# Optimization experiments

Hardware: AMD Instinct MI355X
Metric: run time of the kernel (lower is better)

The kernel has to match this reference:

```python
import jax, jax.numpy as jnp
import numpy as np

C = 1024          # analysis_channels
K = 2             # encoder kernel_size
DILATIONS = (1, 2, 4, 8, 16, 32, 64, 1)
N_EVENTS = 16
N_FREQS = 16
NEG_SLOPE = 0.2   # leaky_relu slope
B, T = 64, 128    # batch, spectrogram frames (n_samples=2**15, hop 256)
WINIT = 0.05      # exp.init_weights uniform(-0.05, 0.05)
POS_CH = 2 * N_FREQS + 1  # 33


def setup_inputs() -> dict:
    key = jax.random.key(0)
    ks = jax.random.split(key, 8)
    u = lambda k, shape: jax.random.uniform(k, shape, jnp.float32, -WINIT, WINIT)
    return {
        'x': jax.random.normal(ks[0], (B, C, T), jnp.float32),  # pre-computed spectrogram path
        'w_spec': u(ks[1], (C, C)), 'b_spec': jnp.zeros((C,), jnp.float32),
        'w_pos': u(ks[2], (C, POS_CH)), 'b_pos': jnp.zeros((C,), jnp.float32),
        'enc_w': u(ks[3], (len(DILATIONS), C, C, K)), 'enc_b': jnp.zeros((len(DILATIONS), C), jnp.float32),
        'w_vec': u(ks[4], (C, C)), 'b_vec': jnp.zeros((C,), jnp.float32),
        'w_sw': u(ks[5], (1, C)), 'b_sw': jnp.zeros((1,), jnp.float32),
        'w_par': u(ks[6], (57, C)), 'b_par': jnp.zeros((57,), jnp.float32),
    }


def _pos_encoded(batch, time):
    # [ramp, sin(2^i * ramp), cos(2^i * ramp) for i in range(16)] -> 33 channels
    pos = jnp.linspace(-1.0, 1.0, time)[:, None]
    feats = [pos]
    for i in range(N_FREQS):
        feats.append(jnp.sin((2.0 ** i) * pos))
        feats.append(jnp.cos((2.0 ** i) * pos))
    p = jnp.concatenate(feats, axis=-1).T  # [33, T]
    return jnp.broadcast_to(p[None], (batch, POS_CH, time))


def _forward(x, w_spec, b_spec, w_pos, b_pos, enc_w, enc_b,
             w_vec, b_vec, w_sw, b_sw, w_par, b_par):
    batch, _, time = x.shape
    pos = _pos_encoded(batch, time)
    pos = jnp.einsum('oc,bct->bot', w_pos, pos) + b_pos[None, :, None]
    h = jnp.einsum('oc,bct->bot', w_spec, x) + b_spec[None, :, None] + pos

    # AntiCausalStack: residual dilated blocks, right (anti-causal) padding, summed skip outputs
    acc = jnp.zeros_like(h)
    for i, d in enumerate(DILATIONS):
        skip = h
        hp = jnp.pad(h, ((0, 0), (0, 0), (0, d * (K - 1))))  # pad end -> anti-causal
        conv = jax.lax.conv_general_dilated(
            hp, enc_w[i], (1,), [(0, 0)], rhs_dilation=(d,),
            dimension_numbers=('NCH', 'OIH', 'NCH')) + enc_b[i][None, :, None]
        conv = jnp.where(conv >= 0, conv, NEG_SLOPE * conv)  # leaky_relu
        h = conv + skip
        # do_norm=True: unit-norm over channel dim per time step
        h = h / (jnp.linalg.norm(h, axis=1, keepdims=True) + 1e-8)
        acc = acc + h
    encoded = acc

    vecs = jnp.einsum('oc,bct->bot', w_vec, encoded) + b_vec[None, :, None]    # [B,C,T]
    switch = jnp.einsum('oc,bct->bot', w_sw, encoded) + b_sw[None, :, None]    # [B,1,T]
    attn = jnp.abs(switch)[:, 0, :]                                             # [B,T]

    # sparsify + sparsify_vectors: top-k event scores, gather vectors, scale by score
    values, indices = jax.lax.top_k(attn, N_EVENTS)                             # [B,16]
    gathered = jnp.take_along_axis(vecs, indices[:, None, :], axis=2)           # [B,C,16]
    events = gathered.transpose(0, 2, 1) * values[:, :, None]                   # [B,16,C]

    return jnp.einsum('bnc,pc->bnp', events, w_par) + b_par[None, None, :]      # [B,16,57]


def reference(x, w_spec, b_spec, w_pos, b_pos, enc_w, enc_b,
              w_vec, b_vec, w_sw, b_sw, w_par, b_par):
    return _forward(x, w_spec, b_spec, w_pos, b_pos, enc_w, enc_b,
                    w_vec, b_vec, w_sw, b_sw, w_par, b_par)
```

## Files before the change

kernel.cpp:

```cpp
#include <hip/hip_runtime.h>
#include <math.h>

#define kB 64
#define kC 1024
#define kT 128
#define kLayers 8
#define kPos 33
#define kEv 16
#define kPar 57

#define BM 128
#define kOB (kC / BM)
#define BK 16
#define NTHR 256

#define SLAB ((size_t)kB * kC * kT)

typedef __attribute__((ext_vector_type(8))) short short8v;
typedef __attribute__((ext_vector_type(4))) float float4v;
typedef __attribute__((ext_vector_type(4))) unsigned short ushort4v;

__device__ __forceinline__ unsigned short bf_hi(float f) {
    unsigned int x = __float_as_uint(f);
    unsigned int r = x + 0x7fffu + ((x >> 16) & 1u);
    return (unsigned short)(r >> 16);
}
__device__ __forceinline__ float bf_f(unsigned short u) {
    return __uint_as_float(((unsigned int)u) << 16);
}

__global__ void pos_kernel(const float* __restrict__ w_pos,
                           const float* __restrict__ b_pos,
                           float* __restrict__ posproj) {
    int o = blockIdx.x;
    int t = threadIdx.x;
    float ramp = -1.0f + 2.0f * (float)t / (float)(kT - 1);
    const float* wr = w_pos + (size_t)o * kPos;
    float s = b_pos[o] + wr[0] * ramp;
    float p2 = 1.0f;
#pragma unroll
    for (int i = 0; i < 16; ++i) {
        float sv, cv;
        sincosf(p2 * ramp, &sv, &cv);
        s += wr[1 + 2 * i] * sv + wr[2 + 2 * i] * cv;
        p2 *= 2.0f;
    }
    posproj[(size_t)o * kT + t] = s;
}

__global__ void mt_kernel(const float* __restrict__ w_par,
                          const float* __restrict__ w_vec,
                          const float* __restrict__ b_vec,
                          float* __restrict__ Mt,
                          float* __restrict__ pbias) {
    if (blockIdx.x == kPar) {
        int p = threadIdx.x;
        if (p < kPar) {
            float s = 0.f;
            for (int c = 0; c < kC; ++c) s += w_par[(size_t)p * kC + c] * b_vec[c];
            pbias[p] = s;
        }
        return;
    }
    int p = blockIdx.x;
    int k = threadIdx.x * 4;
    float mx = 0.f, my = 0.f, mz = 0.f, mw = 0.f;
    for (int o = 0; o < kC; ++o) {
        float wp = w_par[(size_t)p * kC + o];
        float4 wv = *(const float4*)(w_vec + (size_t)o * kC + k);
        mx += wp * wv.x; my += wp * wv.y; mz += wp * wv.z; mw += wp * wv.w;
    }
    Mt[(size_t)(k + 0) * kPar + p] = mx;
    Mt[(size_t)(k + 1) * kPar + p] = my;
    Mt[(size_t)(k + 2) * kPar + p] = mz;
    Mt[(size_t)(k + 3) * kPar + p] = mw;
}

__global__ __launch_bounds__(NTHR) void spec_gemm(
    const float* __restrict__ x, const float* __restrict__ w_spec,
    const float* __restrict__ b_spec, const float* __restrict__ posproj,
    float* __restrict__ h) {
    __shared__ float As[BK][BM];
    __shared__ float Bs[BK][kT];
    const int obase = blockIdx.x * BM;
    const int b = blockIdx.y;
    const int tid = threadIdx.x;
    const int tx4 = (tid & 15) * 4;
    const int ty4 = (tid >> 4) * 4;
    const float* xb = x + (size_t)b * kC * kT;
    float acc[8][8] = {};

    for (int kc = 0; kc < kC; kc += BK) {
        __syncthreads();
        {
            int oo = tid >> 1;
            int ccb = (tid & 1) * 8;
            const float* wrow = w_spec + (size_t)(obase + oo) * kC + kc + ccb;
            float4 v0 = *(const float4*)(wrow);
            float4 v1 = *(const float4*)(wrow + 4);
            As[ccb + 0][oo] = v0.x; As[ccb + 1][oo] = v0.y;
            As[ccb + 2][oo] = v0.z; As[ccb + 3][oo] = v0.w;
            As[ccb + 4][oo] = v1.x; As[ccb + 5][oo] = v1.y;
            As[ccb + 6][oo] = v1.z; As[ccb + 7][oo] = v1.w;
        }
#pragma unroll
        for (int pass = 0; pass < 2; ++pass) {
            int row = (tid >> 5) + pass * 8;
            int col = (tid & 31) * 4;
            *(float4*)&Bs[row][col] = *(const float4*)(xb + (size_t)(kc + row) * kT + col);
        }
        __syncthreads();
#pragma unroll
        for (int kk = 0; kk < BK; ++kk) {
            float a[8], bb[8];
            *(float4*)&a[0] = *(float4*)&As[kk][ty4];
            *(float4*)&a[4] = *(float4*)&As[kk][64 + ty4];
            *(float4*)&bb[0] = *(float4*)&Bs[kk][tx4];
            *(float4*)&bb[4] = *(float4*)&Bs[kk][64 + tx4];
#pragma unroll
            for (int m = 0; m < 8; ++m)
#pragma unroll
                for (int n = 0; n < 8; ++n) acc[m][n] += a[m] * bb[n];
        }
    }
#pragma unroll
    for (int m = 0; m < 8; ++m) {
        int o = obase + (m < 4 ? ty4 + m : 64 + ty4 + m - 4);
        float bias = b_spec[o];
        const float* pp = posproj + (size_t)o * kT;
        float* hrow = h + ((size_t)b * kC + o) * kT;
#pragma unroll
        for (int half = 0; half < 2; ++half) {
            int t0 = half * 64 + tx4;
            float4 pv = *(const float4*)(pp + t0);
            float4 r;
            r.x = acc[m][half * 4 + 0] + bias + pv.x;
            r.y = acc[m][half * 4 + 1] + bias + pv.y;
            r.z = acc[m][half * 4 + 2] + bias + pv.z;
            r.w = acc[m][half * 4 + 3] + bias + pv.w;
            *(float4*)(hrow + t0) = r;
        }
    }
}

__global__ void wconv_kernel(const float* __restrict__ src,
                             unsigned short* __restrict__ wpl) {
    int o = blockIdx.x;
    int tid = threadIdx.x;
    const float* r = src + (size_t)o * (2 * kC) + tid * 8;
    float4 v0 = *(const float4*)r;
    float4 v1 = *(const float4*)(r + 4);
    float t0v[4] = {v0.x, v0.z, v1.x, v1.z};
    float t1v[4] = {v0.y, v0.w, v1.y, v1.w};
    int c0 = tid * 4;
    ushort4v h0, l0, h1, l1;
#pragma unroll
    for (int j = 0; j < 4; ++j) {
        unsigned short h = bf_hi(t0v[j]); h0[j] = h; l0[j] = bf_hi(t0v[j] - bf_f(h));
        unsigned short g = bf_hi(t1v[j]); h1[j] = g; l1[j] = bf_hi(t1v[j] - bf_f(g));
    }
    size_t base = (size_t)o * kC + c0;
    const size_t P = (size_t)kC * kC;
    *(ushort4v*)&wpl[base] = h0;
    *(ushort4v*)&wpl[base + P] = h1;
    *(ushort4v*)&wpl[base + 2 * P] = l0;
    *(ushort4v*)&wpl[base + 3 * P] = l1;
}

template <int DIL>
__global__ __launch_bounds__(NTHR, 2) void conv_mfma(
    const unsigned short* __restrict__ tpl,
    const unsigned short* __restrict__ wpl,
    const float* __restrict__ bconv,
    float* __restrict__ hpre,
    float* __restrict__ ssp) {
    __shared__ short Asl[2 * 128 * 64];
    __shared__ short Bsl[192 * 64];
    __shared__ float red[1024];
    const int tid = threadIdx.x;
    const int obase = blockIdx.x * BM;
    const int b = blockIdx.y;
    const int lane = tid & 63;
    const int w = tid >> 6;
    const int r16 = lane & 15;
    const int kq = lane >> 4;
    const int mrow = (w & 1) * 64;
    const int ncol = (w >> 1) * 64;
    const size_t PW = (size_t)kC * kC;

    float4v acc[4][4];
#pragma unroll
    for (int m = 0; m < 4; ++m)
#pragma unroll
        for (int n = 0; n < 4; ++n) {
            float4v z = {0.f, 0.f, 0.f, 0.f};
            acc[m][n] = z;
        }

    {
        short8v z = {0, 0, 0, 0, 0, 0, 0, 0};
#pragma unroll
        for (int r = 0; r < 2; ++r) {
            int cw = r * 256 + tid;
            int t = 128 + (cw >> 3);
            int g = cw & 7;
            *(short8v*)&Bsl[t * 64 + ((g ^ (t & 7)) << 3)] = z;
        }
    }

    for (int kc = 0; kc < kC; kc += 32) {
        __syncthreads();
#pragma unroll
        for (int r = 0; r < 8; ++r) {
            int cw = r * 256 + tid;
            int g = cw & 7;
            int o = (cw >> 3) & 127;
            int tap = cw >> 10;
            size_t src = ((size_t)((g & 1) * 2 + tap) * kC + (obase + o)) * kC + kc + ((g >> 1) << 3);
            short8v v = *(const short8v*)&wpl[src];
            *(short8v*)&Asl[tap * 8192 + o * 64 + ((g ^ (o & 7)) << 3)] = v;
        }
#pragma unroll
        for (int r = 0; r < 4; ++r) {
            int cw = r * 256 + tid;
            int g = cw & 7;
            int t = cw >> 3;
            size_t src = (size_t)(g & 1) * SLAB + ((size_t)b * kT + t) * kC + kc + ((g >> 1) << 3);
            short8v v = *(const short8v*)&tpl[src];
            *(short8v*)&Bsl[t * 64 + ((g ^ (t & 7)) << 3)] = v;
        }
        __syncthreads();
#pragma unroll
        for (int tap = 0; tap < 2; ++tap) {
            short8v ah[4], al[4], bh[4], bl[4];
#pragma unroll
            for (int m = 0; m < 4; ++m) {
                int ol = mrow + m * 16 + r16;
                const short* rowp = &Asl[tap * 8192 + ol * 64];
                ah[m] = *(const short8v*)&rowp[(((kq << 1)) ^ (ol & 7)) << 3];
                al[m] = *(const short8v*)&rowp[(((kq << 1) | 1) ^ (ol & 7)) << 3];
            }
#pragma unroll
            for (int n = 0; n < 4; ++n) {
                int tr = ncol + n * 16 + r16 + tap * DIL;
                const short* rowp = &Bsl[tr * 64];
                bh[n] = *(const short8v*)&rowp[(((kq << 1)) ^ (tr & 7)) << 3];
                bl[n] = *(const short8v*)&rowp[(((kq << 1) | 1) ^ (tr & 7)) << 3];
            }
#pragma unroll
            for (int m = 0; m < 4; ++m)
#pragma unroll
                for (int n = 0; n < 4; ++n) {
                    acc[m][n] = __builtin_amdgcn_mfma_f32_16x16x32_bf16(ah[m], bh[n], acc[m][n], 0, 0, 0);
                    acc[m][n] = __builtin_amdgcn_mfma_f32_16x16x32_bf16(ah[m], bl[n], acc[m][n], 0, 0, 0);
                    acc[m][n] = __builtin_amdgcn_mfma_f32_16x16x32_bf16(al[m], bh[n], acc[m][n], 0, 0, 0);
                }
        }
    }

    const unsigned short* thi = tpl;
    const unsigned short* tlo = tpl + SLAB;
    float sn[4] = {0.f, 0.f, 0.f, 0.f};
#pragma unroll
    for (int m = 0; m < 4; ++m) {
        int ob4 = obase + mrow + m * 16 + kq * 4;
        float4v bias = *(const float4v*)&bconv[ob4];
#pragma unroll
        for (int n = 0; n < 4; ++n) {
            int t = ncol + n * 16 + r16;
            size_t sidx = ((size_t)b * kT + t) * kC + ob4;
            ushort4v sh = *(const ushort4v*)&thi[sidx];
            ushort4v sl = *(const ushort4v*)&tlo[sidx];
#pragma unroll
            for (int j = 0; j < 4; ++j) {
                float v = acc[m][n][j] + bias[j];
                v = v >= 0.f ? v : 0.2f * v;
                float hp = v + bf_f(sh[j]) + bf_f(sl[j]);
                hpre[((size_t)b * kC + ob4 + j) * kT + t] = hp;
                sn[n] += hp * hp;
            }
        }
    }
#pragma unroll
    for (int n = 0; n < 4; ++n)
        red[w * 256 + kq * 64 + n * 16 + r16] = sn[n];
    __syncthreads();
    if (tid < kT) {
        int t = tid;
        int base = (t < 64) ? 0 : 2;
        int tl = t & 63;
        float s = 0.f;
#pragma unroll
        for (int ww = 0; ww < 2; ++ww)
#pragma unroll
            for (int q = 0; q < 4; ++q)
                s += red[(base + ww) * 256 + q * 64 + tl];
        ssp[((size_t)blockIdx.x * kB + b) * kT + t] = s;
    }
}

__global__ void normfac(const float* __restrict__ ssp, float* __restrict__ rn) {
    int b = blockIdx.x;
    int t = threadIdx.x;
    float s = 0.f;
#pragma unroll
    for (int j = 0; j < kOB; ++j) s += ssp[((size_t)j * kB + b) * kT + t];
    rn[b * kT + t] = 1.0f / (sqrtf(s) + 1e-8f);
}

template <int MODE>
__global__ void trans_kernel(const float* __restrict__ hsrc,
                             const float* __restrict__ rn,
                             float* __restrict__ acc,
                             unsigned short* __restrict__ tpl,
                             int first) {
    __shared__ float tile[64][68];
    int b = blockIdx.x;
    int c0 = blockIdx.y * 64;
    int t0 = blockIdx.z * 64;
    int tid = threadIdx.x;
#pragma unroll
    for (int r = 0; r < 4; ++r) {
        int row = r * 16 + (tid >> 4);
        int col = (tid & 15) * 4;
        size_t idx = ((size_t)b * kC + c0 + row) * kT + t0 + col;
        float4 v = *(const float4*)&hsrc[idx];
        if constexpr (MODE) {
            float4 rv = *(const float4*)&rn[b * kT + t0 + col];
            v.x *= rv.x; v.y *= rv.y; v.z *= rv.z; v.w *= rv.w;
            if (first) {
                *(float4*)&acc[idx] = v;
            } else {
                float4 a = *(const float4*)&acc[idx];
                a.x += v.x; a.y += v.y; a.z += v.z; a.w += v.w;
                *(float4*)&acc[idx] = a;
            }
        }
        *(float4*)&tile[row][col] = v;
    }
    __syncthreads();
    unsigned short* thi = tpl;
    unsigned short* tlo = tpl + SLAB;
#pragma unroll
    for (int r = 0; r < 2; ++r) {
        int trow = r * 32 + (tid >> 3);
        int cc = (tid & 7) * 8;
        short8v hp, lp;
#pragma unroll
        for (int j = 0; j < 8; ++j) {
            float f = tile[cc + j][trow];
            unsigned short h = bf_hi(f);
            hp[j] = (short)h;
            lp[j] = (short)bf_hi(f - bf_f(h));
        }
        size_t dst = ((size_t)b * kT + t0 + trow) * kC + c0 + cc;
        *(short8v*)&thi[dst] = hp;
        *(short8v*)&tlo[dst] = lp;
    }
}

__global__ void switch_partial(const float* __restrict__ acc,
                               const float* __restrict__ w_sw,
                               float* __restrict__ swp) {
    int b = blockIdx.x;
    int cblk = blockIdx.y;
    int t = threadIdx.x & 127;
    int half = threadIdx.x >> 7;
    int cbase = cblk * 128 + half * 64;
    const float* arow = acc + ((size_t)b * kC + cbase) * kT + t;
    float p = 0.f;
    for (int j = 0; j < 64; ++j) p += w_sw[cbase + j] * arow[(size_t)j * kT];
    __shared__ float red2[2][128];
    red2[half][t] = p;
    __syncthreads();
    if (half == 0)
        swp[((size_t)cblk * kB + b) * kT + t] = red2[0][t] + red2[1][t];
}

__global__ void topk_kernel(const float* __restrict__ swp,
                            const float* __restrict__ b_sw,
                            float* __restrict__ vals, int* __restrict__ idxs) {
    int b = blockIdx.x;
    int t = threadIdx.x;
    __shared__ float cur[128];
    __shared__ float rv[128];
    __shared__ int ri[128];
    {
        float s = b_sw[0];
#pragma unroll
        for (int j = 0; j < kC / 128; ++j)
            s += swp[((size_t)j * kB + b) * kT + t];
        cur[t] = fabsf(s);
    }
    __syncthreads();
    for (int r = 0; r < kEv; ++r) {
        rv[t] = cur[t];
        ri[t] = t;
        __syncthreads();
        for (int s = 64; s >= 1; s >>= 1) {
            if (t < s) {
                float v2 = rv[t + s];
                int i2 = ri[t + s];
                if (v2 > rv[t] || (v2 == rv[t] && i2 < ri[t])) { rv[t] = v2; ri[t] = i2; }
            }
            __syncthreads();
        }
        if (t == 0) {
            vals[b * kEv + r] = rv[0];
            idxs[b * kEv + r] = ri[0];
            cur[ri[0]] = -1.0f;
        }
        __syncthreads();
    }
}

__global__ void final_kernel(const float* __restrict__ acc,
                             const float* __restrict__ Mt,
                             const float* __restrict__ pbias,
                             const float* __restrict__ b_par,
                             const float* __restrict__ vals,
                             const int* __restrict__ idxs,
                             float* __restrict__ out) {
    int bn = blockIdx.x;
    int b = bn >> 4;
    int tid = threadIdx.x;
    __shared__ float gs[kC];
    __shared__ float redf[4][64];
    int idx = idxs[bn];
    float val = vals[bn];
#pragma unroll
    for (int j = 0; j < 4; ++j) {
        int k = tid * 4 + j;
        gs[k] = acc[((size_t)b * kC + k) * kT + idx];
    }
    __syncthreads();
    int kg = tid >> 6;
    int pp = tid & 63;
    float partial = 0.f;
    if (pp < kPar) {
        for (int j = 0; j < 256; ++j) {
            int k = kg * 256 + j;
            partial += Mt[(size_t)k * kPar + pp] * gs[k];
        }
    }
    redf[kg][pp] = partial;
    __syncthreads();
    if (kg == 0 && pp < kPar) {
        float s = redf[0][pp] + redf[1][pp] + redf[2][pp] + redf[3][pp];
        out[(size_t)bn * kPar + pp] = val * (s + pbias[pp]) + b_par[pp];
    }
}

extern "C" void kernel_launch(void* const* d_in, const int* in_sizes, int n_in,
                              void* d_out, int out_size, void* d_ws, size_t ws_size,
                              hipStream_t stream) {
    (void)in_sizes; (void)n_in; (void)out_size; (void)ws_size;
    const float* x      = (const float*)d_in[0];
    const float* w_spec = (const float*)d_in[1];
    const float* b_spec = (const float*)d_in[2];
    const float* w_pos  = (const float*)d_in[3];
    const float* b_pos  = (const float*)d_in[4];
    const float* enc_w  = (const float*)d_in[5];
    const float* enc_b  = (const float*)d_in[6];
    const float* w_vec  = (const float*)d_in[7];
    const float* b_vec  = (const float*)d_in[8];
    const float* w_sw   = (const float*)d_in[9];
    const float* b_sw   = (const float*)d_in[10];
    const float* w_par  = (const float*)d_in[11];
    const float* b_par  = (const float*)d_in[12];
    float* out = (float*)d_out;

    float* hpre = (float*)d_ws;
    float* acc  = hpre + SLAB;
    unsigned short* tpl = (unsigned short*)(acc + SLAB);
    unsigned short* wpl = tpl + 2 * SLAB;
    float* posproj = (float*)(wpl + (size_t)4 * kC * kC);
    float* ssp   = posproj + (size_t)kC * kT;
    float* rnorm = ssp + (size_t)kOB * kB * kT;
    float* swp   = rnorm + (size_t)kB * kT;
    float* vals  = swp + (size_t)kOB * kB * kT;
    int*   idxs  = (int*)(vals + kB * kEv);
    float* Mt    = (float*)(idxs + kB * kEv);
    float* pbias = Mt + (size_t)kC * kPar;

    pos_kernel<<<kC, kT, 0, stream>>>(w_pos, b_pos, posproj);
    mt_kernel<<<kPar + 1, 256, 0, stream>>>(w_par, w_vec, b_vec, Mt, pbias);
    spec_gemm<<<dim3(kC / BM, kB), NTHR, 0, stream>>>(x, w_spec, b_spec, posproj, hpre);
    trans_kernel<0><<<dim3(kB, kC / 64, kT / 64), NTHR, 0, stream>>>(
        hpre, rnorm, acc, tpl, 0);

    const int dils[kLayers] = {1, 2, 4, 8, 16, 32, 64, 1};
    for (int i = 0; i < kLayers; ++i) {
        const float* wi = enc_w + (size_t)i * kC * kC * 2;
        const float* bi = enc_b + (size_t)i * kC;
        wconv_kernel<<<kC, NTHR, 0, stream>>>(wi, wpl);
        dim3 grid(kC / BM, kB);
        switch (dils[i]) {
            case 1:  conv_mfma<1><<<grid, NTHR, 0, stream>>>(tpl, wpl, bi, hpre, ssp); break;
            case 2:  conv_mfma<2><<<grid, NTHR, 0, stream>>>(tpl, wpl, bi, hpre, ssp); break;
            case 4:  conv_mfma<4><<<grid, NTHR, 0, stream>>>(tpl, wpl, bi, hpre, ssp); break;
            case 8:  conv_mfma<8><<<grid, NTHR, 0, stream>>>(tpl, wpl, bi, hpre, ssp); break;
            case 16: conv_mfma<16><<<grid, NTHR, 0, stream>>>(tpl, wpl, bi, hpre, ssp); break;
            case 32: conv_mfma<32><<<grid, NTHR, 0, stream>>>(tpl, wpl, bi, hpre, ssp); break;
            case 64: conv_mfma<64><<<grid, NTHR, 0, stream>>>(tpl, wpl, bi, hpre, ssp); break;
        }
        normfac<<<kB, kT, 0, stream>>>(ssp, rnorm);
        trans_kernel<1><<<dim3(kB, kC / 64, kT / 64), NTHR, 0, stream>>>(
            hpre, rnorm, acc, tpl, i == 0 ? 1 : 0);
    }

    switch_partial<<<dim3(kB, kC / 128), 256, 0, stream>>>(acc, w_sw, swp);
    topk_kernel<<<kB, 128, 0, stream>>>(swp, b_sw, vals, idxs);
    final_kernel<<<kB * kEv, 256, 0, stream>>>(acc, Mt, pbias, b_par, vals, idxs, out);
}
```

Measured before the change: 1.537 ms.

## Fuse per-layer normalization and transpose into conv epilogue with deferred norm scaling

Removes the per-layer trans_kernel by having each conv kernel write its un-normalized output directly in the split-bf16 transposed layout. The previous layer's norm factor is applied lazily, by scaling the two tap accumulators and the skip term separately with the factor at t and at t+DIL. The accumulation of normalized outputs moves into the conv epilogue, with a final accfin kernel adding the last layer. The input spectrogram GEMM moves from FP32 FMA to split-bf16 MFMA with a preceding transpose/convert kernel. This cuts full-tensor FP32 round trips per layer. In exchange it adds two accumulator sets per thread (more register pressure) and strided scattered accumulator writes in the epilogue.

```diff
diff --git a/kernel.cpp b/kernel.cpp
--- a/kernel.cpp
+++ b/kernel.cpp
@@ -11,7 +11,6 @@
 
 #define BM 128
 #define kOB (kC / BM)
-#define BK 16
 #define NTHR 256
 
 #define SLAB ((size_t)kB * kC * kT)
@@ -76,73 +75,6 @@
     Mt[(size_t)(k + 3) * kPar + p] = mw;
 }
 
-__global__ __launch_bounds__(NTHR) void spec_gemm(
-    const float* __restrict__ x, const float* __restrict__ w_spec,
-    const float* __restrict__ b_spec, const float* __restrict__ posproj,
-    float* __restrict__ h) {
-    __shared__ float As[BK][BM];
-    __shared__ float Bs[BK][kT];
-    const int obase = blockIdx.x * BM;
-    const int b = blockIdx.y;
-    const int tid = threadIdx.x;
-    const int tx4 = (tid & 15) * 4;
-    const int ty4 = (tid >> 4) * 4;
-    const float* xb = x + (size_t)b * kC * kT;
-    float acc[8][8] = {};
-
-    for (int kc = 0; kc < kC; kc += BK) {
-        __syncthreads();
-        {
-            int oo = tid >> 1;
-            int ccb = (tid & 1) * 8;
-            const float* wrow = w_spec + (size_t)(obase + oo) * kC + kc + ccb;
-            float4 v0 = *(const float4*)(wrow);
-            float4 v1 = *(const float4*)(wrow + 4);
-            As[ccb + 0][oo] = v0.x; As[ccb + 1][oo] = v0.y;
-            As[ccb + 2][oo] = v0.z; As[ccb + 3][oo] = v0.w;
-            As[ccb + 4][oo] = v1.x; As[ccb + 5][oo] = v1.y;
-            As[ccb + 6][oo] = v1.z; As[ccb + 7][oo] = v1.w;
-        }
-#pragma unroll
-        for (int pass = 0; pass < 2; ++pass) {
-            int row = (tid >> 5) + pass * 8;
-            int col = (tid & 31) * 4;
-            *(float4*)&Bs[row][col] = *(const float4*)(xb + (size_t)(kc + row) * kT + col);
-        }
-        __syncthreads();
-#pragma unroll
-        for (int kk = 0; kk < BK; ++kk) {
-            float a[8], bb[8];
-            *(float4*)&a[0] = *(float4*)&As[kk][ty4];
-            *(float4*)&a[4] = *(float4*)&As[kk][64 + ty4];
-            *(float4*)&bb[0] = *(float4*)&Bs[kk][tx4];
-            *(float4*)&bb[4] = *(float4*)&Bs[kk][64 + tx4];
-#pragma unroll
-            for (int m = 0; m < 8; ++m)
-#pragma unroll
-                for (int n = 0; n < 8; ++n) acc[m][n] += a[m] * bb[n];
-        }
-    }
-#pragma unroll
-    for (int m = 0; m < 8; ++m) {
-        int o = obase + (m < 4 ? ty4 + m : 64 + ty4 + m - 4);
-        float bias = b_spec[o];
-        const float* pp = posproj + (size_t)o * kT;
-        float* hrow = h + ((size_t)b * kC + o) * kT;
-#pragma unroll
-        for (int half = 0; half < 2; ++half) {
-            int t0 = half * 64 + tx4;
-            float4 pv = *(const float4*)(pp + t0);
-            float4 r;
-            r.x = acc[m][half * 4 + 0] + bias + pv.x;
-            r.y = acc[m][half * 4 + 1] + bias + pv.y;
-            r.z = acc[m][half * 4 + 2] + bias + pv.z;
-            r.w = acc[m][half * 4 + 3] + bias + pv.w;
-            *(float4*)(hrow + t0) = r;
-        }
-    }
-}
-
 __global__ void wconv_kernel(const float* __restrict__ src,
                              unsigned short* __restrict__ wpl) {
     int o = blockIdx.x;
@@ -167,13 +99,165 @@
     *(ushort4v*)&wpl[base + 3 * P] = l1;
 }
 
-template <int DIL>
+__global__ void wspec_kernel(const float* __restrict__ src,
+                             unsigned short* __restrict__ wsp) {
+    int o = blockIdx.x;
+    int c0 = threadIdx.x * 4;
+    float4 v = *(const float4*)(src + (size_t)o * kC + c0);
+    float f[4] = {v.x, v.y, v.z, v.w};
+    ushort4v hh, ll;
+#pragma unroll
+    for (int j = 0; j < 4; ++j) {
+        unsigned short h = bf_hi(f[j]); hh[j] = h; ll[j] = bf_hi(f[j] - bf_f(h));
+    }
+    size_t base = (size_t)o * kC + c0;
+    *(ushort4v*)&wsp[base] = hh;
+    *(ushort4v*)&wsp[base + (size_t)kC * kC] = ll;
+}
+
+__global__ void trans0_kernel(const float* __restrict__ hsrc,
+                              unsigned short* __restrict__ tpl) {
+    __shared__ float tile[64][68];
+    int b = blockIdx.x;
+    int c0 = blockIdx.y * 64;
+    int t0 = blockIdx.z * 64;
+    int tid = threadIdx.x;
+#pragma unroll
+    for (int r = 0; r < 4; ++r) {
+        int row = r * 16 + (tid >> 4);
+        int col = (tid & 15) * 4;
+        size_t idx = ((size_t)b * kC + c0 + row) * kT + t0 + col;
+        float4 v = *(const float4*)&hsrc[idx];
+        *(float4*)&tile[row][col] = v;
+    }
+    __syncthreads();
+    unsigned short* thi = tpl;
+    unsigned short* tlo = tpl + SLAB;
+#pragma unroll
+    for (int r = 0; r < 2; ++r) {
+        int trow = r * 32 + (tid >> 3);
+        int cc = (tid & 7) * 8;
+        short8v hp, lp;
+#pragma unroll
+        for (int j = 0; j < 8; ++j) {
+            float f = tile[cc + j][trow];
+            unsigned short h = bf_hi(f);
+            hp[j] = (short)h;
+            lp[j] = (short)bf_hi(f - bf_f(h));
+        }
+        size_t dst = ((size_t)b * kT + t0 + trow) * kC + c0 + cc;
+        *(short8v*)&thi[dst] = hp;
+        *(short8v*)&tlo[dst] = lp;
+    }
+}
+
+__global__ __launch_bounds__(NTHR, 2) void spec_mfma(
+    const unsigned short* __restrict__ xt,
+    const unsigned short* __restrict__ wsp,
+    const float* __restrict__ b_spec,
+    const float* __restrict__ posproj,
+    unsigned short* __restrict__ tplo) {
+    __shared__ short Asl[128 * 64];
+    __shared__ short Bsl[128 * 64];
+    const int tid = threadIdx.x;
+    const int obase = blockIdx.x * BM;
+    const int b = blockIdx.y;
+    const int lane = tid & 63;
+    const int w = tid >> 6;
+    const int r16 = lane & 15;
+    const int kq = lane >> 4;
+    const int mrow = (w & 1) * 64;
+    const int ncol = (w >> 1) * 64;
+
+    float4v acc[4][4];
+#pragma unroll
+    for (int m = 0; m < 4; ++m)
+#pragma unroll
+        for (int n = 0; n < 4; ++n) {
+            float4v z = {0.f, 0.f, 0.f, 0.f};
+            acc[m][n] = z;
+        }
+
+    for (int kc = 0; kc < kC; kc += 32) {
+        __syncthreads();
+#pragma unroll
+        for (int r = 0; r < 4; ++r) {
+            int cw = r * 256 + tid;
+            int g = cw & 7;
+            int o = cw >> 3;
+            size_t src = ((size_t)(g & 1) * kC + (obase + o)) * kC + kc + ((g >> 1) << 3);
+            short8v v = *(const short8v*)&wsp[src];
+            *(short8v*)&Asl[o * 64 + ((g ^ (o & 7)) << 3)] = v;
+        }
+#pragma unroll
+        for (int r = 0; r < 4; ++r) {
+            int cw = r * 256 + tid;
+            int g = cw & 7;
+            int t = cw >> 3;
+            size_t src = (size_t)(g & 1) * SLAB + ((size_t)b * kT + t) * kC + kc + ((g >> 1) << 3);
+            short8v v = *(const short8v*)&xt[src];
+            *(short8v*)&Bsl[t * 64 + ((g ^ (t & 7)) << 3)] = v;
+        }
+        __syncthreads();
+        short8v ah[4], al[4], bh[4], bl[4];
+#pragma unroll
+        for (int m = 0; m < 4; ++m) {
+            int ol = mrow + m * 16 + r16;
+            const short* rowp = &Asl[ol * 64];
+            ah[m] = *(const short8v*)&rowp[(((kq << 1)) ^ (ol & 7)) << 3];
+            al[m] = *(const short8v*)&rowp[(((kq << 1) | 1) ^ (ol & 7)) << 3];
+        }
+#pragma unroll
+        for (int n = 0; n < 4; ++n) {
+            int tr = ncol + n * 16 + r16;
+            const short* rowp = &Bsl[tr * 64];
+            bh[n] = *(const short8v*)&rowp[(((kq << 1)) ^ (tr & 7)) << 3];
+            bl[n] = *(const short8v*)&rowp[(((kq << 1) | 1) ^ (tr & 7)) << 3];
+        }
+#pragma unroll
+        for (int m = 0; m < 4; ++m)
+#pragma unroll
+            for (int n = 0; n < 4; ++n) {
+                acc[m][n] = __builtin_amdgcn_mfma_f32_16x16x32_bf16(ah[m], bh[n], acc[m][n], 0, 0, 0);
+                acc[m][n] = __builtin_amdgcn_mfma_f32_16x16x32_bf16(ah[m], bl[n], acc[m][n], 0, 0, 0);
+                acc[m][n] = __builtin_amdgcn_mfma_f32_16x16x32_bf16(al[m], bh[n], acc[m][n], 0, 0, 0);
+            }
+    }
+
+    unsigned short* thi = tplo;
+    unsigned short* tlo = tplo + SLAB;
+#pragma unroll
+    for (int m = 0; m < 4; ++m) {
+        int ob4 = obase + mrow + m * 16 + kq * 4;
+        float4v bias = *(const float4v*)&b_spec[ob4];
+#pragma unroll
+        for (int n = 0; n < 4; ++n) {
+            int t = ncol + n * 16 + r16;
+            ushort4v hh, hl;
+#pragma unroll
+            for (int j = 0; j < 4; ++j) {
+                float v = acc[m][n][j] + bias[j] + posproj[(size_t)(ob4 + j) * kT + t];
+                unsigned short h = bf_hi(v);
+                hh[j] = h;
+                hl[j] = bf_hi(v - bf_f(h));
+            }
+            size_t sidx = ((size_t)b * kT + t) * kC + ob4;
+            *(ushort4v*)&thi[sidx] = hh;
+            *(ushort4v*)&tlo[sidx] = hl;
+        }
+    }
+}
+
+template <int DIL, int FIRST>
 __global__ __launch_bounds__(NTHR, 2) void conv_mfma(
-    const unsigned short* __restrict__ tpl,
+    const unsigned short* __restrict__ tpli,
     const unsigned short* __restrict__ wpl,
     const float* __restrict__ bconv,
-    float* __restrict__ hpre,
-    float* __restrict__ ssp) {
+    const float* __restrict__ rn,
+    unsigned short* __restrict__ tplo,
+    float* __restrict__ ssp,
+    float* __restrict__ accp,
+    int accmode) {
     __shared__ short Asl[2 * 128 * 64];
     __shared__ short Bsl[192 * 64];
     __shared__ float red[1024];
@@ -186,15 +270,15 @@
     const int kq = lane >> 4;
     const int mrow = (w & 1) * 64;
     const int ncol = (w >> 1) * 64;
-    const size_t PW = (size_t)kC * kC;
-
-    float4v acc[4][4];
+
+    float4v acc0[4][4], acc1[4][4];
 #pragma unroll
     for (int m = 0; m < 4; ++m)
 #pragma unroll
         for (int n = 0; n < 4; ++n) {
             float4v z = {0.f, 0.f, 0.f, 0.f};
-            acc[m][n] = z;
+            acc0[m][n] = z;
+            acc1[m][n] = z;
         }
 
     {
@@ -226,23 +310,22 @@
             int g = cw & 7;
             int t = cw >> 3;
             size_t src = (size_t)(g & 1) * SLAB + ((size_t)b * kT + t) * kC + kc + ((g >> 1) << 3);
-            short8v v = *(const short8v*)&tpl[src];
+            short8v v = *(const short8v*)&tpli[src];
             *(short8v*)&Bsl[t * 64 + ((g ^ (t & 7)) << 3)] = v;
         }
         __syncthreads();
-#pragma unroll
-        for (int tap = 0; tap < 2; ++tap) {
+        {
             short8v ah[4], al[4], bh[4], bl[4];
 #pragma unroll
             for (int m = 0; m < 4; ++m) {
                 int ol = mrow + m * 16 + r16;
-                const short* rowp = &Asl[tap * 8192 + ol * 64];
+                const short* rowp = &Asl[ol * 64];
                 ah[m] = *(const short8v*)&rowp[(((kq << 1)) ^ (ol & 7)) << 3];
                 al[m] = *(const short8v*)&rowp[(((kq << 1) | 1) ^ (ol & 7)) << 3];
             }
 #pragma unroll
             for (int n = 0; n < 4; ++n) {
-                int tr = ncol + n * 16 + r16 + tap * DIL;
+                int tr = ncol + n * 16 + r16;
                 const short* rowp = &Bsl[tr * 64];
                 bh[n] = *(const short8v*)&rowp[(((kq << 1)) ^ (tr & 7)) << 3];
                 bl[n] = *(const short8v*)&rowp[(((kq << 1) | 1) ^ (tr & 7)) << 3];
@@ -251,15 +334,42 @@
             for (int m = 0; m < 4; ++m)
 #pragma unroll
                 for (int n = 0; n < 4; ++n) {
-                    acc[m][n] = __builtin_amdgcn_mfma_f32_16x16x32_bf16(ah[m], bh[n], acc[m][n], 0, 0, 0);
-                    acc[m][n] = __builtin_amdgcn_mfma_f32_16x16x32_bf16(ah[m], bl[n], acc[m][n], 0, 0, 0);
-                    acc[m][n] = __builtin_amdgcn_mfma_f32_16x16x32_bf16(al[m], bh[n], acc[m][n], 0, 0, 0);
+                    acc0[m][n] = __builtin_amdgcn_mfma_f32_16x16x32_bf16(ah[m], bh[n], acc0[m][n], 0, 0, 0);
+                    acc0[m][n] = __builtin_amdgcn_mfma_f32_16x16x32_bf16(ah[m], bl[n], acc0[m][n], 0, 0, 0);
+                    acc0[m][n] = __builtin_amdgcn_mfma_f32_16x16x32_bf16(al[m], bh[n], acc0[m][n], 0, 0, 0);
                 }
         }
-    }
-
-    const unsigned short* thi = tpl;
-    const unsigned short* tlo = tpl + SLAB;
+        {
+            short8v ah[4], al[4], bh[4], bl[4];
+#pragma unroll
+            for (int m = 0; m < 4; ++m) {
+                int ol = mrow + m * 16 + r16;
+                const short* rowp = &Asl[8192 + ol * 64];
+                ah[m] = *(const short8v*)&rowp[(((kq << 1)) ^ (ol & 7)) << 3];
+                al[m] = *(const short8v*)&rowp[(((kq << 1) | 1) ^ (ol & 7)) << 3];
+            }
+#pragma unroll
+            for (int n = 0; n < 4; ++n) {
+                int tr = ncol + n * 16 + r16 + DIL;
+                const short* rowp = &Bsl[tr * 64];
+                bh[n] = *(const short8v*)&rowp[(((kq << 1)) ^ (tr & 7)) << 3];
+                bl[n] = *(const short8v*)&rowp[(((kq << 1) | 1) ^ (tr & 7)) << 3];
+            }
+#pragma unroll
+            for (int m = 0; m < 4; ++m)
+#pragma unroll
+                for (int n = 0; n < 4; ++n) {
+                    acc1[m][n] = __builtin_amdgcn_mfma_f32_16x16x32_bf16(ah[m], bh[n], acc1[m][n], 0, 0, 0);
+                    acc1[m][n] = __builtin_amdgcn_mfma_f32_16x16x32_bf16(ah[m], bl[n], acc1[m][n], 0, 0, 0);
+                    acc1[m][n] = __builtin_amdgcn_mfma_f32_16x16x32_bf16(al[m], bh[n], acc1[m][n], 0, 0, 0);
+                }
+        }
+    }
+
+    const unsigned short* phi = tpli;
+    const unsigned short* plo = tpli + SLAB;
+    unsigned short* ohi = tplo;
+    unsigned short* olo = tplo + SLAB;
     float sn[4] = {0.f, 0.f, 0.f, 0.f};
 #pragma unroll
     for (int m = 0; m < 4; ++m) {
@@ -268,17 +378,35 @@
 #pragma unroll
         for (int n = 0; n < 4; ++n) {
             int t = ncol + n * 16 + r16;
+            float rt, rt1;
+            if (FIRST) {
+                rt = 1.0f; rt1 = 1.0f;
+            } else {
+                rt = rn[b * kT + t];
+                rt1 = (t + DIL < kT) ? rn[b * kT + t + DIL] : 0.0f;
+            }
             size_t sidx = ((size_t)b * kT + t) * kC + ob4;
-            ushort4v sh = *(const ushort4v*)&thi[sidx];
-            ushort4v sl = *(const ushort4v*)&tlo[sidx];
+            ushort4v sh = *(const ushort4v*)&phi[sidx];
+            ushort4v sl = *(const ushort4v*)&plo[sidx];
+            ushort4v hh, hl;
 #pragma unroll
             for (int j = 0; j < 4; ++j) {
-                float v = acc[m][n][j] + bias[j];
+                float v = rt * acc0[m][n][j] + rt1 * acc1[m][n][j] + bias[j];
                 v = v >= 0.f ? v : 0.2f * v;
-                float hp = v + bf_f(sh[j]) + bf_f(sl[j]);
-                hpre[((size_t)b * kC + ob4 + j) * kT + t] = hp;
+                float skip = rt * (bf_f(sh[j]) + bf_f(sl[j]));
+                float hp = v + skip;
                 sn[n] += hp * hp;
-            }
+                unsigned short h = bf_hi(hp);
+                hh[j] = h;
+                hl[j] = bf_hi(hp - bf_f(h));
+                if (accmode == 1) {
+                    accp[((size_t)b * kC + ob4 + j) * kT + t] = skip;
+                } else if (accmode == 2) {
+                    accp[((size_t)b * kC + ob4 + j) * kT + t] += skip;
+                }
+            }
+            *(ushort4v*)&ohi[sidx] = hh;
+            *(ushort4v*)&olo[sidx] = hl;
         }
     }
 #pragma unroll
@@ -299,67 +427,56 @@
     }
 }
 
-__global__ void normfac(const float* __restrict__ ssp, float* __restrict__ rn) {
+__global__ void normfac(const float* __restrict__ ssp, float* __restrict__ rnv) {
     int b = blockIdx.x;
     int t = threadIdx.x;
     float s = 0.f;
 #pragma unroll
     for (int j = 0; j < kOB; ++j) s += ssp[((size_t)j * kB + b) * kT + t];
-    rn[b * kT + t] = 1.0f / (sqrtf(s) + 1e-8f);
-}
-
-template <int MODE>
-__global__ void trans_kernel(const float* __restrict__ hsrc,
-                             const float* __restrict__ rn,
-                             float* __restrict__ acc,
-                             unsigned short* __restrict__ tpl,
-                             int first) {
-    __shared__ float tile[64][68];
+    rnv[b * kT + t] = 1.0f / (sqrtf(s) + 1e-8f);
+}
+
+__global__ void accfin(const unsigned short* __restrict__ tpl,
+                       const float* __restrict__ rnv,
+                       float* __restrict__ accp) {
+    __shared__ float tile[64][65];
     int b = blockIdx.x;
     int c0 = blockIdx.y * 64;
     int t0 = blockIdx.z * 64;
     int tid = threadIdx.x;
+    const unsigned short* thi = tpl;
+    const unsigned short* tlo = tpl + SLAB;
+    {
+        int tr = tid >> 2;
+        int cc = (tid & 3) * 16;
+        float rt = rnv[b * kT + t0 + tr];
+        size_t src = ((size_t)b * kT + t0 + tr) * kC + c0 + cc;
+        short8v h0 = *(const short8v*)&thi[src];
+        short8v h1 = *(const short8v*)&thi[src + 8];
+        short8v l0 = *(const short8v*)&tlo[src];
+        short8v l1 = *(const short8v*)&tlo[src + 8];
+#pragma unroll
+        for (int j = 0; j < 8; ++j) {
+            tile[cc + j][tr] = rt * (bf_f((unsigned short)h0[j]) + bf_f((unsigned short)l0[j]));
+            tile[cc + 8 + j][tr] = rt * (bf_f((unsigned short)h1[j]) + bf_f((unsigned short)l1[j]));
+        }
+    }
+    __syncthreads();
 #pragma unroll
     for (int r = 0; r < 4; ++r) {
         int row = r * 16 + (tid >> 4);
         int col = (tid & 15) * 4;
         size_t idx = ((size_t)b * kC + c0 + row) * kT + t0 + col;
-        float4 v = *(const float4*)&hsrc[idx];
-        if constexpr (MODE) {
-            float4 rv = *(const float4*)&rn[b * kT + t0 + col];
-            v.x *= rv.x; v.y *= rv.y; v.z *= rv.z; v.w *= rv.w;
-            if (first) {
-                *(float4*)&acc[idx] = v;
-            } else {
-                float4 a = *(const float4*)&acc[idx];
-                a.x += v.x; a.y += v.y; a.z += v.z; a.w += v.w;
-                *(float4*)&acc[idx] = a;
-            }
-        }
-        *(float4*)&tile[row][col] = v;
-    }
-    __syncthreads();
-    unsigned short* thi = tpl;
-    unsigned short* tlo = tpl + SLAB;
-#pragma unroll
-    for (int r = 0; r < 2; ++r) {
-        int trow = r * 32 + (tid >> 3);
-        int cc = (tid & 7) * 8;
-        short8v hp, lp;
-#pragma unroll
-        for (int j = 0; j < 8; ++j) {
-            float f = tile[cc + j][trow];
-            unsigned short h = bf_hi(f);
-            hp[j] = (short)h;
-            lp[j] = (short)bf_hi(f - bf_f(h));
-        }
-        size_t dst = ((size_t)b * kT + t0 + trow) * kC + c0 + cc;
-        *(short8v*)&thi[dst] = hp;
-        *(short8v*)&tlo[dst] = lp;
-    }
-}
-
-__global__ void switch_partial(const float* __restrict__ acc,
+        float4 a = *(const float4*)&accp[idx];
+        a.x += tile[row][col + 0];
+        a.y += tile[row][col + 1];
+        a.z += tile[row][col + 2];
+        a.w += tile[row][col + 3];
+        *(float4*)&accp[idx] = a;
+    }
+}
+
+__global__ void switch_partial(const float* __restrict__ accp,
                                const float* __restrict__ w_sw,
                                float* __restrict__ swp) {
     int b = blockIdx.x;
@@ -367,7 +484,7 @@
     int t = threadIdx.x & 127;
     int half = threadIdx.x >> 7;
     int cbase = cblk * 128 + half * 64;
-    const float* arow = acc + ((size_t)b * kC + cbase) * kT + t;
+    const float* arow = accp + ((size_t)b * kC + cbase) * kT + t;
     float p = 0.f;
     for (int j = 0; j < 64; ++j) p += w_sw[cbase + j] * arow[(size_t)j * kT];
     __shared__ float red2[2][128];
@@ -414,7 +531,7 @@
     }
 }
 
-__global__ void final_kernel(const float* __restrict__ acc,
+__global__ void final_kernel(const float* __restrict__ accp,
                              const float* __restrict__ Mt,
                              const float* __restrict__ pbias,
                              const float* __restrict__ b_par,
@@ -431,7 +548,7 @@
 #pragma unroll
     for (int j = 0; j < 4; ++j) {
         int k = tid * 4 + j;
-        gs[k] = acc[((size_t)b * kC + k) * kT + idx];
+        gs[k] = accp[((size_t)b * kC + k) * kT + idx];
     }
     __syncthreads();
     int kg = tid >> 6;
@@ -470,14 +587,15 @@
     const float* b_par  = (const float*)d_in[12];
     float* out = (float*)d_out;
 
-    float* hpre = (float*)d_ws;
-    float* acc  = hpre + SLAB;
-    unsigned short* tpl = (unsigned short*)(acc + SLAB);
-    unsigned short* wpl = tpl + 2 * SLAB;
-    float* posproj = (float*)(wpl + (size_t)4 * kC * kC);
+    unsigned short* tplA = (unsigned short*)d_ws;
+    unsigned short* tplB = tplA + 2 * SLAB;
+    float* acc  = (float*)(tplB + 2 * SLAB);
+    unsigned short* wpl = (unsigned short*)(acc + SLAB);
+    unsigned short* wsp = wpl + (size_t)4 * kC * kC;
+    float* posproj = (float*)(wsp + (size_t)2 * kC * kC);
     float* ssp   = posproj + (size_t)kC * kT;
-    float* rnorm = ssp + (size_t)kOB * kB * kT;
-    float* swp   = rnorm + (size_t)kB * kT;
+    float* rnv   = ssp + (size_t)kOB * kB * kT;
+    float* swp   = rnv + (size_t)kB * kT;
     float* vals  = swp + (size_t)kOB * kB * kT;
     int*   idxs  = (int*)(vals + kB * kEv);
     float* Mt    = (float*)(idxs + kB * kEv);
@@ -485,29 +603,37 @@
 
     pos_kernel<<<kC, kT, 0, stream>>>(w_pos, b_pos, posproj);
     mt_kernel<<<kPar + 1, 256, 0, stream>>>(w_par, w_vec, b_vec, Mt, pbias);
-    spec_gemm<<<dim3(kC / BM, kB), NTHR, 0, stream>>>(x, w_spec, b_spec, posproj, hpre);
-    trans_kernel<0><<<dim3(kB, kC / 64, kT / 64), NTHR, 0, stream>>>(
-        hpre, rnorm, acc, tpl, 0);
+    wspec_kernel<<<kC, 256, 0, stream>>>(w_spec, wsp);
+    trans0_kernel<<<dim3(kB, kC / 64, kT / 64), NTHR, 0, stream>>>(x, tplB);
+    spec_mfma<<<dim3(kC / BM, kB), NTHR, 0, stream>>>(tplB, wsp, b_spec, posproj, tplA);
 
     const int dils[kLayers] = {1, 2, 4, 8, 16, 32, 64, 1};
+    unsigned short* cur = tplA;
+    unsigned short* nxt = tplB;
     for (int i = 0; i < kLayers; ++i) {
         const float* wi = enc_w + (size_t)i * kC * kC * 2;
         const float* bi = enc_b + (size_t)i * kC;
-        wconv_kernel<<<kC, NTHR, 0, stream>>>(wi, wpl);
+        int am = (i == 0) ? 0 : (i == 1 ? 1 : 2);
+        wconv_kernel<<<kC, 256, 0, stream>>>(wi, wpl);
         dim3 grid(kC / BM, kB);
-        switch (dils[i]) {
-            case 1:  conv_mfma<1><<<grid, NTHR, 0, stream>>>(tpl, wpl, bi, hpre, ssp); break;
-            case 2:  conv_mfma<2><<<grid, NTHR, 0, stream>>>(tpl, wpl, bi, hpre, ssp); break;
-            case 4:  conv_mfma<4><<<grid, NTHR, 0, stream>>>(tpl, wpl, bi, hpre, ssp); break;
-            case 8:  conv_mfma<8><<<grid, NTHR, 0, stream>>>(tpl, wpl, bi, hpre, ssp); break;
-            case 16: conv_mfma<16><<<grid, NTHR, 0, stream>>>(tpl, wpl, bi, hpre, ssp); break;
-            case 32: conv_mfma<32><<<grid, NTHR, 0, stream>>>(tpl, wpl, bi, hpre, ssp); break;
-            case 64: conv_mfma<64><<<grid, NTHR, 0, stream>>>(tpl, wpl, bi, hpre, ssp); break;
-        }
-        normfac<<<kB, kT, 0, stream>>>(ssp, rnorm);
-        trans_kernel<1><<<dim3(kB, kC / 64, kT / 64), NTHR, 0, stream>>>(
-            hpre, rnorm, acc, tpl, i == 0 ? 1 : 0);
-    }
+        if (i == 0) {
+            conv_mfma<1, 1><<<grid, NTHR, 0, stream>>>(cur, wpl, bi, rnv, nxt, ssp, acc, am);
+        } else {
+            switch (dils[i]) {
+                case 1:  conv_mfma<1, 0><<<grid, NTHR, 0, stream>>>(cur, wpl, bi, rnv, nxt, ssp, acc, am); break;
+                case 2:  conv_mfma<2, 0><<<grid, NTHR, 0, stream>>>(cur, wpl, bi, rnv, nxt, ssp, acc, am); break;
+                case 4:  conv_mfma<4, 0><<<grid, NTHR, 0, stream>>>(cur, wpl, bi, rnv, nxt, ssp, acc, am); break;
+                case 8:  conv_mfma<8, 0><<<grid, NTHR, 0, stream>>>(cur, wpl, bi, rnv, nxt, ssp, acc, am); break;
+                case 16: conv_mfma<16, 0><<<grid, NTHR, 0, stream>>>(cur, wpl, bi, rnv, nxt, ssp, acc, am); break;
+                case 32: conv_mfma<32, 0><<<grid, NTHR, 0, stream>>>(cur, wpl, bi, rnv, nxt, ssp, acc, am); break;
+                case 64: conv_mfma<64, 0><<<grid, NTHR, 0, stream>>>(cur, wpl, bi, rnv, nxt, ssp, acc, am); break;
+            }
+        }
+        normfac<<<kB, kT, 0, stream>>>(ssp, rnv);
+        unsigned short* tmp = cur; cur = nxt; nxt = tmp;
+    }
+
+    accfin<<<dim3(kB, kC / 64, kT / 64), NTHR, 0, stream>>>(cur, rnv, acc);
 
     switch_partial<<<dim3(kB, kC / 128), 256, 0, stream>>>(acc, w_sw, swp);
     topk_kernel<<<kB, 128, 0, stream>>>(swp, b_sw, vals, idxs);
```

Result: slower. 1.652 ms (+7.5%).
